# Kernel optimization log

Hardware: AMD Instinct MI355X
Metric: run time of the kernel (lower is better)

Reference implementation:

```python
import jax, jax.numpy as jnp
import numpy as np

# ---- static configuration (matches init_kwargs / input_specs) ----
B, N = 4, 128            # images, proposals per image
C = 256                  # feature channels (in_channels)
HF, WF = 23, 30          # feature map size (input 736x960 / 32)
PH, PW = 7, 7            # pooled_size
SCALE = 1.0 / 32.0       # scale_factor
HIMG, WIMG = HF * 32, WF * 32
KH = HF // PH + 2        # max rows any pooling bin can span
KW = WF // PW + 2        # max cols any pooling bin can span
HID, OUT = 256, 5
NEG = -1e30


def _roi_pool_one(f, box):
    """Quantized ROI max pooling for one proposal.
    f: (C, HF, WF) feature map; box: (4,) [x1,y1,x2,y2] in feature coords.
    Returns (C, PH, PW)."""
    box = jax.lax.stop_gradient(box)  # indices are non-differentiable
    x1 = jnp.clip(jnp.floor(box[0]).astype(jnp.int32), 0, WF - 1)
    y1 = jnp.clip(jnp.floor(box[1]).astype(jnp.int32), 0, HF - 1)
    roi_w = jnp.clip(jnp.ceil(box[2]).astype(jnp.int32) - x1, 1, WF)
    roi_h = jnp.clip(jnp.ceil(box[3]).astype(jnp.int32) - y1, 1, HF)
    ph = jnp.arange(PH)
    pw = jnp.arange(PW)
    hs = y1 + (ph * roi_h) // PH                       # bin row starts (PH,)
    he = y1 + ((ph + 1) * roi_h + PH - 1) // PH        # bin row ends (ceil)
    ws = x1 + (pw * roi_w) // PW
    we = x1 + ((pw + 1) * roi_w + PW - 1) // PW
    hidx = hs[:, None] + jnp.arange(KH)[None, :]       # (PH, KH)
    hval = (hidx < he[:, None]) & (hidx < HF)
    widx = ws[:, None] + jnp.arange(KW)[None, :]       # (PW, KW)
    wval = (widx < we[:, None]) & (widx < WF)
    rows = f[:, jnp.clip(hidx, 0, HF - 1), :]          # (C, PH, KH, WF) gather
    rmax = jnp.max(jnp.where(hval[None, :, :, None], rows, NEG), axis=2)  # (C, PH, WF)
    cols = rmax[:, :, jnp.clip(widx, 0, WF - 1)]       # (C, PH, PW, KW) gather
    return jnp.max(jnp.where(wval[None, None], cols, NEG), axis=3)        # (C, PH, PW)


# vmap over proposals, then over images: (B,C,HF,WF),(B,N,4) -> (B,N,C,PH,PW)
_roi_pool = jax.vmap(jax.vmap(_roi_pool_one, in_axes=(None, 0)), in_axes=(0, 0))


def setup_inputs() -> dict:
    key = jax.random.key(0)
    ks = jax.random.split(key, 8)
    features = jax.random.normal(ks[0], (B, C, HF, WF), jnp.float32)
    # valid proposals in image coordinates (min box side ~32 px)
    x1 = jax.random.uniform(ks[1], (B, N)) * (WIMG - 32.0)
    y1 = jax.random.uniform(ks[2], (B, N)) * (HIMG - 32.0)
    x2 = x1 + 32.0 + jax.random.uniform(ks[3], (B, N)) * (WIMG - 32.0 - x1)
    y2 = y1 + 32.0 + jax.random.uniform(ks[4], (B, N)) * (HIMG - 32.0 - y1)
    conf = jax.random.normal(ks[5], (B, N))
    proposals = jnp.stack([x1, y1, x2, y2, conf], axis=-1)  # (B, N, 5)
    W1 = jax.random.normal(ks[6], (HID, C * PH * PW), jnp.float32) * 0.01
    b1 = jnp.zeros((HID,), jnp.float32)
    W2 = jax.random.normal(ks[7], (OUT, HID), jnp.float32) * 0.01
    b2 = jnp.zeros((OUT,), jnp.float32)
    return {"features": features, "proposals": proposals,
            "W1": W1, "b1": b1, "W2": W2, "b2": b2}


def reference(features, proposals, W1, b1, W2, b2):
    boxes_feat = proposals[..., :4] * SCALE                 # image -> feature coords
    pooled = _roi_pool(features, boxes_feat)                # (B, N, C, PH, PW)
    flat = pooled.reshape(B, N, C * PH * PW)
    h = jax.nn.relu(jnp.einsum('bnf,hf->bnh', flat, W1) + b1)
    out = jnp.einsum('bnh,oh->bno', h, W2) + b2             # (B, N, 5)
    refined_boxes = proposals[..., :4] + out[..., :4]
    refined_conf = jax.nn.sigmoid(proposals[..., 4:5] + out[..., 4:5])
    return jnp.concatenate([refined_boxes, refined_conf], axis=-1)  # (B, N, 5)
```

## Files before the change

### kernel.cpp

```cpp
#include <hip/hip_runtime.h>
#include <math.h>

#define Bq 4
#define Nq 128
#define Cq 256
#define HFq 23
#define WFq 30
#define PHq 7
#define PWq 7
#define HIDq 256
#define OUTq 5
#define Fq (Cq*PHq*PWq)
#define Mq (Bq*Nq)
#define HWq (HFq*WFq)
#define SCALEq (1.0f/32.0f)
#define NEGq (-1e30f)
#define KHq 5
#define KWq 6
#define SPLITK 14
#define KCH (Fq/SPLITK)
#define KSTEPS (KCH/32)

typedef float f32x4 __attribute__((ext_vector_type(4)));
typedef __bf16 bf16x8 __attribute__((ext_vector_type(8)));
typedef unsigned short u16x8 __attribute__((ext_vector_type(8)));

__device__ __forceinline__ unsigned short f2b(float f) {
    unsigned int u = __float_as_uint(f);
    unsigned int r = (u + 0x7FFFu + ((u >> 16) & 1u)) >> 16;
    return (unsigned short)r;
}

__global__ __launch_bounds__(256) void k_prep(const float* __restrict__ feat,
                                              unsigned short* __restrict__ ft,
                                              const float* __restrict__ W1,
                                              unsigned short* __restrict__ w1p,
                                              float* __restrict__ h) {
    __shared__ __align__(16) unsigned short smem[Fq];
    int bid = blockIdx.x;
    int tid = threadIdx.x;
    if (bid < 704) {
        float (*t)[33] = (float (*)[33])smem;
        int bb  = bid / 176;
        int rem = bid % 176;
        int x0 = (rem % 22) * 32;
        int c0 = (rem / 22) * 32;
        int tx = tid & 31, ty = tid >> 5;
        const float* src = feat + (size_t)bb * Cq * HWq;
        unsigned short* dst = ft + (size_t)bb * HWq * Cq;
#pragma unroll
        for (int i = 0; i < 4; ++i) {
            int c = c0 + ty + i * 8;
            int x = x0 + tx;
            if (x < HWq) t[ty + i * 8][tx] = src[(size_t)c * HWq + x];
        }
        __syncthreads();
        int u = tid & 15, xl = tid >> 4;
#pragma unroll
        for (int i = 0; i < 2; ++i) {
            int xloc = xl + i * 16;
            int x = x0 + xloc;
            if (x < HWq) {
                ushort2 o;
                o.x = f2b(t[u * 2][xloc]);
                o.y = f2b(t[u * 2 + 1][xloc]);
                *(ushort2*)(dst + (size_t)x * Cq + c0 + u * 2) = o;
            }
        }
    } else if (bid < 960) {
        int j = bid - 704;
        const float4* src = (const float4*)(W1 + (size_t)j * Fq);
        for (int i = tid; i < Fq / 4; i += 256) {
            float4 v = src[i];
            ushort4 o;
            o.x = f2b(v.x); o.y = f2b(v.y); o.z = f2b(v.z); o.w = f2b(v.w);
            ((ushort4*)smem)[i] = o;
        }
        __syncthreads();
        uint4* dst = (uint4*)(w1p + (size_t)j * Fq);
        for (int i = tid; i < Fq / 8; i += 256) {
            int base = i * 8;
            int cell = base >> 8;
            int c0v = base & 255;
            unsigned short tmp[8];
#pragma unroll
            for (int u2 = 0; u2 < 8; ++u2) tmp[u2] = smem[(c0v + u2) * 49 + cell];
            dst[i] = *(const uint4*)tmp;
        }
    } else {
        f32x4* h4 = (f32x4*)h;
        int base = (bid - 960) * 4096;
        f32x4 z = {0.f, 0.f, 0.f, 0.f};
#pragma unroll
        for (int u2 = 0; u2 < 16; ++u2) h4[base + u2 * 256 + tid] = z;
    }
}

__global__ __launch_bounds__(256) void k_pool(const unsigned short* __restrict__ ft,
                                              const float* __restrict__ props,
                                              unsigned short* __restrict__ pooled) {
    int wave = threadIdx.x >> 6;
    int lane = threadIdx.x & 63;
    int half = lane >> 5;
    int cl = lane & 31;
    int g = blockIdx.y * 4 + wave;
    int m = blockIdx.x;
    int b = m >> 7;
    const float* pr = props + (size_t)m * 5;
    float b0 = pr[0] * SCALEq, b1v = pr[1] * SCALEq;
    float b2v = pr[2] * SCALEq, b3v = pr[3] * SCALEq;
    int x1 = min(max((int)floorf(b0), 0), WFq - 1);
    int y1 = min(max((int)floorf(b1v), 0), HFq - 1);
    int rw = min(max((int)ceilf(b2v) - x1, 1), WFq);
    int rh = min(max((int)ceilf(b3v) - y1, 1), HFq);
    const unsigned short* ftb = ft + (size_t)b * HWq * Cq + cl * 8;
    unsigned short* pm = pooled + (size_t)m * Fq + cl * 8;

    for (int cell = g; cell < PHq * PWq; cell += 8) {
        int ph = cell / 7;
        int pw = cell - ph * 7;
        int hs = y1 + (ph * rh) / PHq;
        int he = min(y1 + ((ph + 1) * rh + PHq - 1) / PHq, HFq);
        int ws = x1 + (pw * rw) / PWq;
        int we = min(x1 + ((pw + 1) * rw + PWq - 1) / PWq, WFq);
        float acc[8];
#pragma unroll
        for (int u = 0; u < 8; ++u) acc[u] = NEGq;
#pragma unroll
        for (int kh = 0; kh < KHq; ++kh) {
            if (hs + kh < he) {
                const unsigned short* rowp = ftb + (size_t)((hs + kh) * WFq) * Cq;
#pragma unroll
                for (int kw2 = 0; kw2 < 3; ++kw2) {
                    int w = ws + kw2 * 2 + half;
                    if (w < we) {
                        u16x8 v = *(const u16x8*)(rowp + (size_t)w * Cq);
#pragma unroll
                        for (int u = 0; u < 8; ++u)
                            acc[u] = fmaxf(acc[u], __uint_as_float((unsigned)v[u] << 16));
                    }
                }
            }
        }
#pragma unroll
        for (int u = 0; u < 8; ++u) acc[u] = fmaxf(acc[u], __shfl_xor(acc[u], 32));
        if (half == 0) {
            u16x8 o;
#pragma unroll
            for (int u = 0; u < 8; ++u) o[u] = f2b(acc[u]);
            *(u16x8*)(pm + (size_t)cell * Cq) = o;
        }
    }
}

__global__ __launch_bounds__(256) void k_gemm1(const unsigned short* __restrict__ pooled,
                                               const unsigned short* __restrict__ w1p,
                                               float* __restrict__ h) {
    __shared__ __align__(16) unsigned short As[2][64 * 32];
    __shared__ __align__(16) unsigned short Bs[2][64 * 32];
    int m0 = blockIdx.x * 64;
    int j0 = blockIdx.y * 64;
    int kz = blockIdx.z;
    int tid = threadIdx.x;
    int r = tid >> 2, qq = tid & 3;
    const uint4* ap = (const uint4*)(pooled + (size_t)(m0 + r) * Fq + (size_t)kz * KCH + qq * 8);
    const uint4* bp = (const uint4*)(w1p + (size_t)(j0 + r) * Fq + (size_t)kz * KCH + qq * 8);
    int lane = tid & 63, wv = tid >> 6;
    int q = lane >> 4, mr = lane & 15;
    f32x4 acc0 = {0.f, 0.f, 0.f, 0.f};
    f32x4 acc1 = {0.f, 0.f, 0.f, 0.f};
    f32x4 acc2 = {0.f, 0.f, 0.f, 0.f};
    f32x4 acc3 = {0.f, 0.f, 0.f, 0.f};
    int stoff = r * 32 + qq * 8;
    int aoff = (wv * 16 + mr) * 32 + q * 8;
    int boff = mr * 32 + q * 8;

    uint4 av = ap[0];
    uint4 bv = bp[0];
    *(uint4*)(As[0] + stoff) = av;
    *(uint4*)(Bs[0] + stoff) = bv;
    av = ap[4];
    bv = bp[4];
#pragma unroll 2
    for (int s = 0; s < KSTEPS; ++s) {
        __syncthreads();
        int cur = s & 1;
        if (s + 1 < KSTEPS) {
            *(uint4*)(As[cur ^ 1] + stoff) = av;
            *(uint4*)(Bs[cur ^ 1] + stoff) = bv;
            if (s + 2 < KSTEPS) {
                av = ap[(s + 2) * 4];
                bv = bp[(s + 2) * 4];
            }
        }
        bf16x8 a = *(const bf16x8*)(As[cur] + aoff);
        acc0 = __builtin_amdgcn_mfma_f32_16x16x32_bf16(a, *(const bf16x8*)(Bs[cur] + boff),            acc0, 0, 0, 0);
        acc1 = __builtin_amdgcn_mfma_f32_16x16x32_bf16(a, *(const bf16x8*)(Bs[cur] + boff + 16 * 32), acc1, 0, 0, 0);
        acc2 = __builtin_amdgcn_mfma_f32_16x16x32_bf16(a, *(const bf16x8*)(Bs[cur] + boff + 32 * 32), acc2, 0, 0, 0);
        acc3 = __builtin_amdgcn_mfma_f32_16x16x32_bf16(a, *(const bf16x8*)(Bs[cur] + boff + 48 * 32), acc3, 0, 0, 0);
    }
    int mb = m0 + wv * 16 + q * 4;
    int jj = j0 + mr;
#pragma unroll
    for (int r2 = 0; r2 < 4; ++r2) {
        float* row = h + (size_t)(mb + r2) * HIDq + jj;
        atomicAdd(row + 0,  acc0[r2]);
        atomicAdd(row + 16, acc1[r2]);
        atomicAdd(row + 32, acc2[r2]);
        atomicAdd(row + 48, acc3[r2]);
    }
}

__global__ __launch_bounds__(256) void k_tail(const float* __restrict__ h,
                                              const float* __restrict__ b1,
                                              const float* __restrict__ W2,
                                              const float* __restrict__ b2,
                                              const float* __restrict__ props,
                                              float* __restrict__ out) {
    __shared__ float red[OUTq][4];
    int m = blockIdx.x, j = threadIdx.x;
    float hv = fmaxf(h[(size_t)m * HIDq + j] + b1[j], 0.f);
    float p[OUTq];
#pragma unroll
    for (int o = 0; o < OUTq; ++o) p[o] = hv * W2[(size_t)o * HIDq + j];
    int lane = j & 63, wid = j >> 6;
#pragma unroll
    for (int o = 0; o < OUTq; ++o) {
        float v = p[o];
        v += __shfl_xor(v, 1);
        v += __shfl_xor(v, 2);
        v += __shfl_xor(v, 4);
        v += __shfl_xor(v, 8);
        v += __shfl_xor(v, 16);
        v += __shfl_xor(v, 32);
        if (lane == 0) red[o][wid] = v;
    }
    __syncthreads();
    if (j < OUTq) {
        float s = red[j][0] + red[j][1] + red[j][2] + red[j][3] + b2[j];
        float pv = props[(size_t)m * 5 + j];
        float r;
        if (j < 4) r = pv + s;
        else r = 1.f / (1.f + expf(-(pv + s)));
        out[(size_t)m * 5 + j] = r;
    }
}

extern "C" void kernel_launch(void* const* d_in, const int* in_sizes, int n_in,
                              void* d_out, int out_size, void* d_ws, size_t ws_size,
                              hipStream_t stream) {
    const float* feat  = (const float*)d_in[0];
    const float* props = (const float*)d_in[1];
    const float* W1    = (const float*)d_in[2];
    const float* b1    = (const float*)d_in[3];
    const float* W2    = (const float*)d_in[4];
    const float* b2    = (const float*)d_in[5];
    float* out = (float*)d_out;

    char* ws = (char*)d_ws;
    unsigned short* ft     = (unsigned short*)(ws);
    unsigned short* w1p    = (unsigned short*)(ws + 1413120);
    unsigned short* pooled = (unsigned short*)(ws + 7835648);
    float* h               = (float*)(ws + 20680704);

    k_prep<<<968, 256, 0, stream>>>(feat, ft, W1, w1p, h);
    k_pool<<<dim3(Mq, 2), 256, 0, stream>>>(ft, props, pooled);
    k_gemm1<<<dim3(8, 4, SPLITK), 256, 0, stream>>>(pooled, w1p, h);
    k_tail<<<Mq, 256, 0, stream>>>(h, b1, W2, b2, props, out);
}
```

Baseline: 120.8 us.

## Double GEMM1 k-tile depth to 64 and XOR-swizzle shared memory layout

The k-step in the split-K bf16 MFMA GEMM grows from 32 to 64, so each barrier-separated iteration issues eight MFMAs instead of four and there are half as many __syncthreads. Shared tiles are stored with an XOR swizzle on the 16-byte chunk index, which should avoid LDS bank conflicts on the strided 128-byte rows. In exchange the kernel uses twice the LDS and more registers for prefetch, which may lower occupancy.

```diff
diff --git a/kernel.cpp b/kernel.cpp
--- a/kernel.cpp
+++ b/kernel.cpp
@@ -19,7 +19,8 @@
 #define KWq 6
 #define SPLITK 14
 #define KCH (Fq/SPLITK)
-#define KSTEPS (KCH/32)
+#define BKq 64
+#define KSTEPS (KCH/BKq)
 
 typedef float f32x4 __attribute__((ext_vector_type(4)));
 typedef __bf16 bf16x8 __attribute__((ext_vector_type(8)));
@@ -156,48 +157,62 @@
 __global__ __launch_bounds__(256) void k_gemm1(const unsigned short* __restrict__ pooled,
                                                const unsigned short* __restrict__ w1p,
                                                float* __restrict__ h) {
-    __shared__ __align__(16) unsigned short As[2][64 * 32];
-    __shared__ __align__(16) unsigned short Bs[2][64 * 32];
+    __shared__ __align__(16) unsigned short As[2][64 * BKq];
+    __shared__ __align__(16) unsigned short Bs[2][64 * BKq];
     int m0 = blockIdx.x * 64;
     int j0 = blockIdx.y * 64;
     int kz = blockIdx.z;
     int tid = threadIdx.x;
     int r = tid >> 2, qq = tid & 3;
-    const uint4* ap = (const uint4*)(pooled + (size_t)(m0 + r) * Fq + (size_t)kz * KCH + qq * 8);
-    const uint4* bp = (const uint4*)(w1p + (size_t)(j0 + r) * Fq + (size_t)kz * KCH + qq * 8);
+    const uint4* ap = (const uint4*)(pooled + (size_t)(m0 + r) * Fq + (size_t)kz * KCH) + qq;
+    const uint4* bp = (const uint4*)(w1p + (size_t)(j0 + r) * Fq + (size_t)kz * KCH) + qq;
     int lane = tid & 63, wv = tid >> 6;
     int q = lane >> 4, mr = lane & 15;
     f32x4 acc0 = {0.f, 0.f, 0.f, 0.f};
     f32x4 acc1 = {0.f, 0.f, 0.f, 0.f};
     f32x4 acc2 = {0.f, 0.f, 0.f, 0.f};
     f32x4 acc3 = {0.f, 0.f, 0.f, 0.f};
-    int stoff = r * 32 + qq * 8;
-    int aoff = (wv * 16 + mr) * 32 + q * 8;
-    int boff = mr * 32 + q * 8;
-
-    uint4 av = ap[0];
-    uint4 bv = bp[0];
-    *(uint4*)(As[0] + stoff) = av;
-    *(uint4*)(Bs[0] + stoff) = bv;
-    av = ap[4];
-    bv = bp[4];
-#pragma unroll 2
+    int st1 = r * 8 + ((qq) ^ (r & 7));
+    int st2 = r * 8 + ((qq ^ 4) ^ (r & 7));
+    int sA = (wv * 16 + mr) * 8;
+    int c0k0 = (q) ^ (mr & 7);
+    int c0k1 = (q ^ 4) ^ (mr & 7);
+
+    uint4 a0v = ap[0], a1v = ap[4];
+    uint4 b0v = bp[0], b1v = bp[4];
+    {
+        uint4* aw = (uint4*)As[0];
+        uint4* bw = (uint4*)Bs[0];
+        aw[st1] = a0v; aw[st2] = a1v;
+        bw[st1] = b0v; bw[st2] = b1v;
+    }
+    a0v = ap[8];  a1v = ap[12];
+    b0v = bp[8];  b1v = bp[12];
     for (int s = 0; s < KSTEPS; ++s) {
         __syncthreads();
         int cur = s & 1;
         if (s + 1 < KSTEPS) {
-            *(uint4*)(As[cur ^ 1] + stoff) = av;
-            *(uint4*)(Bs[cur ^ 1] + stoff) = bv;
+            uint4* aw = (uint4*)As[cur ^ 1];
+            uint4* bw = (uint4*)Bs[cur ^ 1];
+            aw[st1] = a0v; aw[st2] = a1v;
+            bw[st1] = b0v; bw[st2] = b1v;
             if (s + 2 < KSTEPS) {
-                av = ap[(s + 2) * 4];
-                bv = bp[(s + 2) * 4];
+                a0v = ap[(s + 2) * 8];     a1v = ap[(s + 2) * 8 + 4];
+                b0v = bp[(s + 2) * 8];     b1v = bp[(s + 2) * 8 + 4];
             }
         }
-        bf16x8 a = *(const bf16x8*)(As[cur] + aoff);
-        acc0 = __builtin_amdgcn_mfma_f32_16x16x32_bf16(a, *(const bf16x8*)(Bs[cur] + boff),            acc0, 0, 0, 0);
-        acc1 = __builtin_amdgcn_mfma_f32_16x16x32_bf16(a, *(const bf16x8*)(Bs[cur] + boff + 16 * 32), acc1, 0, 0, 0);
-        acc2 = __builtin_amdgcn_mfma_f32_16x16x32_bf16(a, *(const bf16x8*)(Bs[cur] + boff + 32 * 32), acc2, 0, 0, 0);
-        acc3 = __builtin_amdgcn_mfma_f32_16x16x32_bf16(a, *(const bf16x8*)(Bs[cur] + boff + 48 * 32), acc3, 0, 0, 0);
+        const bf16x8* Ab = (const bf16x8*)As[cur];
+        const bf16x8* Bb = (const bf16x8*)Bs[cur];
+        bf16x8 a0 = Ab[sA + c0k0];
+        bf16x8 a1 = Ab[sA + c0k1];
+        acc0 = __builtin_amdgcn_mfma_f32_16x16x32_bf16(a0, Bb[(0  + mr) * 8 + c0k0], acc0, 0, 0, 0);
+        acc1 = __builtin_amdgcn_mfma_f32_16x16x32_bf16(a0, Bb[(16 + mr) * 8 + c0k0], acc1, 0, 0, 0);
+        acc2 = __builtin_amdgcn_mfma_f32_16x16x32_bf16(a0, Bb[(32 + mr) * 8 + c0k0], acc2, 0, 0, 0);
+        acc3 = __builtin_amdgcn_mfma_f32_16x16x32_bf16(a0, Bb[(48 + mr) * 8 + c0k0], acc3, 0, 0, 0);
+        acc0 = __builtin_amdgcn_mfma_f32_16x16x32_bf16(a1, Bb[(0  + mr) * 8 + c0k1], acc0, 0, 0, 0);
+        acc1 = __builtin_amdgcn_mfma_f32_16x16x32_bf16(a1, Bb[(16 + mr) * 8 + c0k1], acc1, 0, 0, 0);
+        acc2 = __builtin_amdgcn_mfma_f32_16x16x32_bf16(a1, Bb[(32 + mr) * 8 + c0k1], acc2, 0, 0, 0);
+        acc3 = __builtin_amdgcn_mfma_f32_16x16x32_bf16(a1, Bb[(48 + mr) * 8 + c0k1], acc3, 0, 0, 0);
     }
     int mb = m0 + wv * 16 + q * 4;
     int jj = j0 + mr;
```

After: 119.7 us. No clear change (-0.9%).
